# Kernel tuning notes

Measured on AMD Instinct MI355X. Metric: run time of the kernel, lower is better.

Reference implementation:

```python
import jax, jax.numpy as jnp
import numpy as np
import math

D_MODEL = 1024
D_STATE = 16
D_CONV = 4
EXPAND = 2
D_INNER = EXPAND * D_MODEL  # 2048
DT_RANK = math.ceil(D_MODEL / 16)  # 64
BATCH = 4
SEQLEN = 4096


def setup_inputs() -> dict:
    key = jax.random.key(0)
    ks = jax.random.split(key, 8)
    sc = lambda d: 1.0 / np.sqrt(d)
    hidden_states = jax.random.normal(ks[0], (BATCH, SEQLEN, D_MODEL), jnp.float32)
    in_proj_w = jax.random.normal(ks[1], (2 * D_INNER, D_MODEL), jnp.float32) * sc(D_MODEL)
    conv_w = jax.random.normal(ks[2], (D_INNER, 1, D_CONV), jnp.float32) * sc(D_CONV)
    conv_b = jnp.zeros((D_INNER,), jnp.float32)
    x_proj_w = jax.random.normal(ks[3], (DT_RANK + 2 * D_STATE, D_INNER), jnp.float32) * sc(D_INNER)
    dt_init_std = DT_RANK ** -0.5
    dt_proj_w = jax.random.uniform(ks[4], (D_INNER, DT_RANK), jnp.float32, -dt_init_std, dt_init_std)
    # dt bias init: inverse-softplus of dt sampled log-uniform in [1e-3, 1e-1]
    dt = jnp.exp(jax.random.uniform(ks[5], (D_INNER,), jnp.float32)
                 * (math.log(0.1) - math.log(0.001)) + math.log(0.001))
    dt = jnp.clip(dt, 1e-4, None)
    dt_proj_b = dt + jnp.log(-jnp.expm1(-dt))
    A_log = jnp.log(jnp.tile(jnp.arange(1, D_STATE + 1, dtype=jnp.float32), (D_INNER, 1)))
    Dp = jnp.ones((D_INNER,), jnp.float32)
    out_proj_w = jax.random.normal(ks[6], (D_MODEL, D_INNER), jnp.float32) * sc(D_INNER)
    return {
        'hidden_states': hidden_states,
        'in_proj_w': in_proj_w,
        'conv_w': conv_w,
        'conv_b': conv_b,
        'x_proj_w': x_proj_w,
        'dt_proj_w': dt_proj_w,
        'dt_proj_b': dt_proj_b,
        'A_log': A_log,
        'D': Dp,
        'out_proj_w': out_proj_w,
    }


def _bimamba_fwd(hidden_states, in_proj_w, conv_w, conv_b, x_proj_w,
                 dt_proj_w, dt_proj_b, A_log, D, out_proj_w):
    Bb, L, _ = hidden_states.shape
    # 1) input projection, split into x and gate z
    xz = hidden_states @ in_proj_w.T                      # (B, L, 2*d_inner)
    x, z = jnp.split(xz, 2, axis=-1)
    # 2) causal depthwise conv1d (torch pads d_conv-1 both sides then truncates
    #    to L, equivalent to left-pad d_conv-1)
    xc = x.transpose(0, 2, 1)                             # (B, d_inner, L)
    xc = jax.lax.conv_general_dilated(
        xc, conv_w, window_strides=(1,), padding=[(D_CONV - 1, 0)],
        dimension_numbers=('NCH', 'OIH', 'NCH'), feature_group_count=D_INNER)
    xc = xc + conv_b[None, :, None]
    x = jax.nn.silu(xc.transpose(0, 2, 1))                # (B, L, d_inner)
    # 3) input-dependent SSM parameters
    x_dbl = x @ x_proj_w.T                                # (B, L, dt_rank + 2*d_state)
    dt, Bm, Cm = jnp.split(x_dbl, [DT_RANK, DT_RANK + D_STATE], axis=-1)
    dt = jax.nn.softplus(dt @ dt_proj_w.T + dt_proj_b)    # (B, L, d_inner)
    A = -jnp.exp(A_log)                                   # (d_inner, d_state)

    # 4) selective scan (faithful to source: einsum 'bdn,bdk->bdk' sums dA over
    #    the state dim n and scales h by that scalar per (b,d))
    def step(h, inp):
        dt_t, B_t, C_t, x_t = inp                         # (B,d),(B,n),(B,n),(B,d)
        dtc = jnp.clip(dt_t, -10.0, 10.0)
        dA = jnp.exp(jnp.clip(dtc[..., None] * A[None], -50.0, 50.0))  # (B,d,n)
        dB_x = dtc[..., None] * B_t[:, None, :] * jnp.clip(x_t, -10.0, 10.0)[..., None]
        h_new = jnp.clip(dA.sum(-1, keepdims=True) * h + dB_x, -100.0, 100.0)
        y_t = (h_new * C_t[:, None, :]).sum(-1)           # (B, d_inner)
        return h_new, y_t

    h0 = jnp.zeros((Bb, D_INNER, D_STATE), x.dtype)
    xs = (dt.transpose(1, 0, 2), Bm.transpose(1, 0, 2),
          Cm.transpose(1, 0, 2), x.transpose(1, 0, 2))
    _, ys = jax.lax.scan(step, h0, xs)                    # ys: (L, B, d_inner)
    y = ys.transpose(1, 0, 2) + x * D[None, None, :]
    # 5) gate + output projection
    y = y * jax.nn.silu(z)
    return y @ out_proj_w.T                               # (B, L, d_model)


def reference(hidden_states, in_proj_w, conv_w, conv_b, x_proj_w,
              dt_proj_w, dt_proj_b, A_log, D, out_proj_w):
    return _bimamba_fwd(hidden_states, in_proj_w, conv_w, conv_b, x_proj_w,
                        dt_proj_w, dt_proj_b, A_log, D, out_proj_w)
```

## Files before the change

kernel.cpp:

```cpp
#include <hip/hip_runtime.h>
#include <math.h>

#define B_   4
#define L_   4096
#define DM   1024
#define DI   2048
#define M_   (B_ * L_)
#define NT   32
#define CH   16
#define NCHUNK (L_ / NT)

typedef unsigned short u16;
typedef unsigned int   u32;
typedef __attribute__((ext_vector_type(8))) short s16x8;
typedef __attribute__((ext_vector_type(4))) float f32x4;

__device__ __forceinline__ float clampf(float v, float lo, float hi) {
    return fminf(fmaxf(v, lo), hi);
}
__device__ __forceinline__ float b2f(u32 u) {
    union { u32 i; float f; } v; v.i = u << 16; return v.f;
}
__device__ __forceinline__ u16 f2b(float f) {
    union { float f; u32 i; } v; v.f = f;
    u32 r = v.i + 0x7FFFu + ((v.i >> 16) & 1u);
    return (u16)(r >> 16);
}
__device__ __forceinline__ float siluf(float x) {
    return x / (1.f + __expf(-x));
}
__device__ __forceinline__ float xor1_add(float x) {
    int t = __builtin_amdgcn_mov_dpp(__float_as_int(x), 0xB1, 0xF, 0xF, true);
    return x + __int_as_float(t);
}
__device__ __forceinline__ float xor2_add(float x) {
    int t = __builtin_amdgcn_mov_dpp(__float_as_int(x), 0x4E, 0xF, 0xF, true);
    return x + __int_as_float(t);
}
__device__ __forceinline__ float mirror8_add(float x) {
    int t = __builtin_amdgcn_mov_dpp(__float_as_int(x), 0x141, 0xF, 0xF, true);
    return x + __int_as_float(t);
}

__global__ __launch_bounds__(256) void gemm_inproj_mfma(
    const float* __restrict__ A, const float* __restrict__ Bw,
    float* __restrict__ X, u16* __restrict__ ZS)
{
    __shared__ u16 Ah[128 * 40], Al[128 * 40], Bh[128 * 40], Bl[128 * 40];
    const int K = 1024;
    const int tid = threadIdx.x;
    const int wid = tid >> 6, lane = tid & 63;
    const int wm = wid >> 1, wn = wid & 1;
    const int lr = lane & 15, lk = (lane >> 4) * 8;
    const long m0 = (long)blockIdx.x * 128;
    const int n0 = blockIdx.y * 128;
    const int srr = tid >> 3;
    const int skk = (tid & 7) * 4;

    f32x4 acc[4][4];
#pragma unroll
    for (int m = 0; m < 4; ++m)
#pragma unroll
        for (int n = 0; n < 4; ++n) acc[m][n] = (f32x4){0.f, 0.f, 0.f, 0.f};

    for (int k0 = 0; k0 < K; k0 += 32) {
        float4 ta[4], tb[4];
#pragma unroll
        for (int v = 0; v < 4; ++v) {
            ta[v] = *(const float4*)&A[(m0 + v * 32 + srr) * K + k0 + skk];
            tb[v] = *(const float4*)&Bw[((long)n0 + v * 32 + srr) * K + k0 + skk];
        }
        __syncthreads();
#pragma unroll
        for (int v = 0; v < 4; ++v) {
            int off = (v * 32 + srr) * 40 + skk;
            ushort4 h, l;
            h.x = f2b(ta[v].x); l.x = f2b(ta[v].x - b2f(h.x));
            h.y = f2b(ta[v].y); l.y = f2b(ta[v].y - b2f(h.y));
            h.z = f2b(ta[v].z); l.z = f2b(ta[v].z - b2f(h.z));
            h.w = f2b(ta[v].w); l.w = f2b(ta[v].w - b2f(h.w));
            *(ushort4*)&Ah[off] = h; *(ushort4*)&Al[off] = l;
            h.x = f2b(tb[v].x); l.x = f2b(tb[v].x - b2f(h.x));
            h.y = f2b(tb[v].y); l.y = f2b(tb[v].y - b2f(h.y));
            h.z = f2b(tb[v].z); l.z = f2b(tb[v].z - b2f(h.z));
            h.w = f2b(tb[v].w); l.w = f2b(tb[v].w - b2f(h.w));
            *(ushort4*)&Bh[off] = h; *(ushort4*)&Bl[off] = l;
        }
        __syncthreads();
        s16x8 ah[4], al[4], bh[4], bl[4];
#pragma unroll
        for (int m = 0; m < 4; ++m) {
            int ro = (wm * 64 + m * 16 + lr) * 40 + lk;
            ah[m] = *(const s16x8*)&Ah[ro];
            al[m] = *(const s16x8*)&Al[ro];
        }
#pragma unroll
        for (int n = 0; n < 4; ++n) {
            int ro = (wn * 64 + n * 16 + lr) * 40 + lk;
            bh[n] = *(const s16x8*)&Bh[ro];
            bl[n] = *(const s16x8*)&Bl[ro];
        }
#pragma unroll
        for (int m = 0; m < 4; ++m)
#pragma unroll
            for (int n = 0; n < 4; ++n) {
                acc[m][n] = __builtin_amdgcn_mfma_f32_16x16x32_bf16(ah[m], bh[n], acc[m][n], 0, 0, 0);
                acc[m][n] = __builtin_amdgcn_mfma_f32_16x16x32_bf16(ah[m], bl[n], acc[m][n], 0, 0, 0);
                acc[m][n] = __builtin_amdgcn_mfma_f32_16x16x32_bf16(al[m], bh[n], acc[m][n], 0, 0, 0);
            }
    }

    const int rbase = (lane >> 4) * 4;
    if (n0 < DI) {
#pragma unroll
        for (int m = 0; m < 4; ++m) {
            long row = m0 + wm * 64 + m * 16 + rbase;
#pragma unroll
            for (int n = 0; n < 4; ++n) {
                int col = n0 + wn * 64 + n * 16 + lr;
#pragma unroll
                for (int ri = 0; ri < 4; ++ri)
                    X[(row + ri) * DI + col] = acc[m][n][ri];
            }
        }
    } else {
#pragma unroll
        for (int m = 0; m < 4; ++m) {
            long row = m0 + wm * 64 + m * 16 + rbase;
#pragma unroll
            for (int n = 0; n < 4; ++n) {
                int col = n0 - DI + wn * 64 + n * 16 + lr;
#pragma unroll
                for (int ri = 0; ri < 4; ++ri)
                    ZS[(row + ri) * DI + col] = f2b(siluf(acc[m][n][ri]));
            }
        }
    }
}

__global__ __launch_bounds__(256) void gemm_outproj_mfma(
    const float* __restrict__ A, const float* __restrict__ Bw,
    float* __restrict__ C)
{
    __shared__ u16 Ah[128 * 40], Bh[128 * 40];
    const int K = 2048;
    const int tid = threadIdx.x;
    const int wid = tid >> 6, lane = tid & 63;
    const int wm = wid >> 1, wn = wid & 1;
    const int lr = lane & 15, lk = (lane >> 4) * 8;
    const long m0 = (long)blockIdx.x * 128;
    const int n0 = blockIdx.y * 128;
    const int srr = tid >> 3;
    const int skk = (tid & 7) * 4;

    f32x4 acc[4][4];
#pragma unroll
    for (int m = 0; m < 4; ++m)
#pragma unroll
        for (int n = 0; n < 4; ++n) acc[m][n] = (f32x4){0.f, 0.f, 0.f, 0.f};

    for (int k0 = 0; k0 < K; k0 += 32) {
        float4 ta[4], tb[4];
#pragma unroll
        for (int v = 0; v < 4; ++v) {
            ta[v] = *(const float4*)&A[(m0 + v * 32 + srr) * K + k0 + skk];
            tb[v] = *(const float4*)&Bw[((long)n0 + v * 32 + srr) * K + k0 + skk];
        }
        __syncthreads();
#pragma unroll
        for (int v = 0; v < 4; ++v) {
            int off = (v * 32 + srr) * 40 + skk;
            ushort4 h;
            h.x = f2b(ta[v].x); h.y = f2b(ta[v].y);
            h.z = f2b(ta[v].z); h.w = f2b(ta[v].w);
            *(ushort4*)&Ah[off] = h;
            h.x = f2b(tb[v].x); h.y = f2b(tb[v].y);
            h.z = f2b(tb[v].z); h.w = f2b(tb[v].w);
            *(ushort4*)&Bh[off] = h;
        }
        __syncthreads();
        s16x8 ah[4], bh[4];
#pragma unroll
        for (int m = 0; m < 4; ++m)
            ah[m] = *(const s16x8*)&Ah[(wm * 64 + m * 16 + lr) * 40 + lk];
#pragma unroll
        for (int n = 0; n < 4; ++n)
            bh[n] = *(const s16x8*)&Bh[(wn * 64 + n * 16 + lr) * 40 + lk];
#pragma unroll
        for (int m = 0; m < 4; ++m)
#pragma unroll
            for (int n = 0; n < 4; ++n)
                acc[m][n] = __builtin_amdgcn_mfma_f32_16x16x32_bf16(ah[m], bh[n], acc[m][n], 0, 0, 0);
    }

    const int rbase = (lane >> 4) * 4;
#pragma unroll
    for (int m = 0; m < 4; ++m) {
        long row = m0 + wm * 64 + m * 16 + rbase;
#pragma unroll
        for (int n = 0; n < 4; ++n) {
            int col = n0 + wn * 64 + n * 16 + lr;
#pragma unroll
            for (int ri = 0; ri < 4; ++ri)
                C[(row + ri) * DM + col] = acc[m][n][ri];
        }
    }
}

__global__ __launch_bounds__(256) void gemm_xproj_conv_mfma(
    const float* __restrict__ X, const float* __restrict__ convw,
    const float* __restrict__ convb, const float* __restrict__ Bw,
    float* __restrict__ C)
{
    const int PITCH = 72;
    __shared__ u16 Ah[64 * PITCH], Al[64 * PITCH];
    __shared__ u16 Bh[96 * PITCH], Bl[96 * PITCH];
    const int tid = threadIdx.x;
    const int wid = tid >> 6, lane = tid & 63;
    const int wm = wid >> 1, wn = wid & 1;
    const int lr = lane & 15, lk = (lane >> 4) * 8;
    const long m0 = (long)blockIdx.x * 64;

    const int rg = tid >> 6;
    const int kk = tid & 63;
    const long gr0 = m0 + rg * 16;
    const int l0r = (int)(gr0 & (L_ - 1));

    f32x4 acc[2][3];
#pragma unroll
    for (int m = 0; m < 2; ++m)
#pragma unroll
        for (int n = 0; n < 3; ++n) acc[m][n] = (f32x4){0.f, 0.f, 0.f, 0.f};

    for (int k0 = 0; k0 < DI; k0 += 64) {
        float4 cwv = *(const float4*)&convw[(k0 + kk) * 4];
        float cbv = convb[k0 + kk];
        float xm3, xm2, xm1;
        if (l0r == 0) { xm3 = 0.f; xm2 = 0.f; xm1 = 0.f; }
        else {
            xm3 = X[(gr0 - 3) * DI + k0 + kk];
            xm2 = X[(gr0 - 2) * DI + k0 + kk];
            xm1 = X[(gr0 - 1) * DI + k0 + kk];
        }
        __syncthreads();
#pragma unroll
// ... 25 lines not shown
            h = f2b(t.w); Bh[off + 3] = h; Bl[off + 3] = f2b(t.w - b2f(h));
        }
        __syncthreads();
#pragma unroll
        for (int kf = 0; kf < 2; ++kf) {
            s16x8 ah[2], al[2], bh[3], bl[3];
#pragma unroll
            for (int m = 0; m < 2; ++m) {
                int ro = (wm * 32 + m * 16 + lr) * PITCH + kf * 32 + lk;
                ah[m] = *(const s16x8*)&Ah[ro];
                al[m] = *(const s16x8*)&Al[ro];
            }
#pragma unroll
            for (int n = 0; n < 3; ++n) {
                int ro = (wn * 48 + n * 16 + lr) * PITCH + kf * 32 + lk;
                bh[n] = *(const s16x8*)&Bh[ro];
                bl[n] = *(const s16x8*)&Bl[ro];
            }
#pragma unroll
            for (int m = 0; m < 2; ++m)
#pragma unroll
                for (int n = 0; n < 3; ++n) {
                    acc[m][n] = __builtin_amdgcn_mfma_f32_16x16x32_bf16(ah[m], bh[n], acc[m][n], 0, 0, 0);
                    acc[m][n] = __builtin_amdgcn_mfma_f32_16x16x32_bf16(ah[m], bl[n], acc[m][n], 0, 0, 0);
                    acc[m][n] = __builtin_amdgcn_mfma_f32_16x16x32_bf16(al[m], bh[n], acc[m][n], 0, 0, 0);
                }
        }
    }

    const int rbase = (lane >> 4) * 4;
#pragma unroll
    for (int m = 0; m < 2; ++m) {
        long row = m0 + wm * 32 + m * 16 + rbase;
#pragma unroll
        for (int n = 0; n < 3; ++n) {
            int col = wn * 48 + n * 16 + lr;
#pragma unroll
            for (int ri = 0; ri < 4; ++ri)
                C[(row + ri) * 96 + col] = acc[m][n][ri];
        }
    }
}

__global__ __launch_bounds__(256, 1) void scan_kernel(
    float* xg, const u16* __restrict__ zsg, const float* __restrict__ xdbl,
    const float* __restrict__ dtw, const float* __restrict__ dtb,
    const float* __restrict__ Dv, const float* __restrict__ convw,
    const float* __restrict__ convb)
{
    __shared__ float sa [3][NT][CH + 1];
    __shared__ float ssv[3][NT][CH + 1];
    __shared__ float sxa[3][NT][CH + 1];
    __shared__ u16   szs[3][NT][CH + 1];
    __shared__ float sbc[3][NT][36];
    __shared__ float sxr[2][NT][CH + 1];
    __shared__ float sdt[2][NT][68];
    __shared__ float scarry[3][CH];
    __shared__ float sg[2][NT][CH + 1];

    const int tid = threadIdx.x;
    const int bb   = blockIdx.x >> 7;
    const int cgrp = blockIdx.x & 127;
    const int d0 = cgrp * CH;
    const long lrow0 = (long)bb * L_;
    const bool producer = (tid >= 128);

    if (producer && (tid - 128) < 3 * CH) {
        int pi = tid - 128;
        scarry[pi >> 4][pi & 15] = 0.f;
    }

    const int p  = tid & 127;
    const int ch = p >> 3, q = p & 7;
    const int d  = d0 + ch;
    float4 cw = {0,0,0,0};
    float cbd = 0.f, dtbd = 0.f, Dd = 0.f;
    float4 wv[16];
    if (producer) {
#pragma unroll
        for (int g = 0; g < 16; ++g)
            wv[g] = *(const float4*)&dtw[(long)d * 64 + 4 * g];
        cw  = *(const float4*)&convw[d * 4];
        cbd = convb[d];
        dtbd = dtb[d];
    } else {
        Dd = Dv[d];
        __builtin_amdgcn_s_setprio(1);
    }
    const int srow = p >> 2, sc4 = (p & 3) * 4;

    auto STAGE = [&](int cc) {
        const long lr0 = lrow0 + (long)cc * NT;
        const int spr = cc & 1, cbn = cc % 3;
        {
            long go = (lr0 + srow) * DI + d0 + sc4;
            float4 xv = *(const float4*)&xg[go];
            sxr[spr][srow][sc4 + 0] = xv.x; sxr[spr][srow][sc4 + 1] = xv.y;
            sxr[spr][srow][sc4 + 2] = xv.z; sxr[spr][srow][sc4 + 3] = xv.w;
            ushort4 zv = *(const ushort4*)&zsg[go];
            szs[cbn][srow][sc4 + 0] = zv.x; szs[cbn][srow][sc4 + 1] = zv.y;
            szs[cbn][srow][sc4 + 2] = zv.z; szs[cbn][srow][sc4 + 3] = zv.w;
        }
#pragma unroll
        for (int v = 0; v < 4; ++v) {
            int idx = p + v * 128;
            int row = idx >> 4, c4 = (idx & 15) * 4;
            float4 t = *(const float4*)&xdbl[(lr0 + row) * 96 + c4];
            *(float4*)&sdt[spr][row][c4] = t;
        }
#pragma unroll
        for (int v = 0; v < 2; ++v) {
            int idx = p + v * 128;
            int row = idx >> 3, sj = idx & 7;
            if (sj < 4) {
                float4 bv = *(const float4*)&xdbl[(lr0 + row) * 96 + 64 + sj * 4];
                sbc[cbn][row][8 * sj + 0] = bv.x; sbc[cbn][row][8 * sj + 2] = bv.y;
                sbc[cbn][row][8 * sj + 4] = bv.z; sbc[cbn][row][8 * sj + 6] = bv.w;
            } else {
                int jj = sj - 4;
                float4 cv = *(const float4*)&xdbl[(lr0 + row) * 96 + 80 + jj * 4];
                sbc[cbn][row][8 * jj + 1] = cv.x; sbc[cbn][row][8 * jj + 3] = cv.y;
                sbc[cbn][row][8 * jj + 5] = cv.z; sbc[cbn][row][8 * jj + 7] = cv.w;
            }
        }
    };

    auto COMPUTE = [&](int cc) {
        const int spr = cc & 1, cbn = cc % 3;
        float xw0, xw1, xw2;
        if (q == 0) { xw0 = scarry[0][ch]; xw1 = scarry[1][ch]; xw2 = scarry[2][ch]; }
        else { xw0 = sxr[spr][4 * q - 3][ch]; xw1 = sxr[spr][4 * q - 2][ch];
               xw2 = sxr[spr][4 * q - 1][ch]; }
        float xw3 = sxr[spr][4 * q + 0][ch];
        float xw4 = sxr[spr][4 * q + 1][ch];
        float xw5 = sxr[spr][4 * q + 2][ch];
        float xw6 = sxr[spr][4 * q + 3][ch];
        sxa[cbn][4 * q + 0][ch] =
            siluf(fmaf(xw0, cw.x, fmaf(xw1, cw.y, fmaf(xw2, cw.z, fmaf(xw3, cw.w, cbd)))));
        sxa[cbn][4 * q + 1][ch] =
            siluf(fmaf(xw1, cw.x, fmaf(xw2, cw.y, fmaf(xw3, cw.z, fmaf(xw4, cw.w, cbd)))));
        sxa[cbn][4 * q + 2][ch] =
            siluf(fmaf(xw2, cw.x, fmaf(xw3, cw.y, fmaf(xw4, cw.z, fmaf(xw5, cw.w, cbd)))));
        sxa[cbn][4 * q + 3][ch] =
            siluf(fmaf(xw3, cw.x, fmaf(xw4, cw.y, fmaf(xw5, cw.z, fmaf(xw6, cw.w, cbd)))));
        if (q == 0) {
            scarry[0][ch] = sxr[spr][NT - 3][ch];
            scarry[1][ch] = sxr[spr][NT - 2][ch];
            scarry[2][ch] = sxr[spr][NT - 1][ch];
        }
#pragma unroll
        for (int j = 0; j < 4; ++j) {
            const int stp = 8 * j + q;
            const float* row = &sdt[spr][stp][0];
            float a0 = 0.f, a1 = 0.f, a2 = 0.f, a3 = 0.f;
#pragma unroll
            for (int g = 0; g < 4; ++g) {
                float4 u0 = *(const float4*)(row + 16 * g + 0);
                float4 u1 = *(const float4*)(row + 16 * g + 4);
                float4 u2 = *(const float4*)(row + 16 * g + 8);
                float4 u3 = *(const float4*)(row + 16 * g + 12);
                float4 w0 = wv[4 * g + 0], w1 = wv[4 * g + 1];
                float4 w2 = wv[4 * g + 2], w3 = wv[4 * g + 3];
                a0 = fmaf(u0.x, w0.x, a0); a0 = fmaf(u0.y, w0.y, a0);
                a0 = fmaf(u0.z, w0.z, a0); a0 = fmaf(u0.w, w0.w, a0);
                a1 = fmaf(u1.x, w1.x, a1); a1 = fmaf(u1.y, w1.y, a1);
                a1 = fmaf(u1.z, w1.z, a1); a1 = fmaf(u1.w, w1.w, a1);
                a2 = fmaf(u2.x, w2.x, a2); a2 = fmaf(u2.y, w2.y, a2);
                a2 = fmaf(u2.z, w2.z, a2); a2 = fmaf(u2.w, w2.w, a2);
                a3 = fmaf(u3.x, w3.x, a3); a3 = fmaf(u3.y, w3.y, a3);
                a3 = fmaf(u3.z, w3.z, a3); a3 = fmaf(u3.w, w3.w, a3);
            }
            float dt = ((a0 + a1) + (a2 + a3)) + dtbd;
            float sp = fmaxf(dt, 0.f) + __logf(1.f + __expf(-fabsf(dt)));
            float dtc = fminf(sp, 10.f);
            float r = __expf(-dtc);
            float r2 = r * r, r4 = r2 * r2, r8 = r4 * r4;
            float a = r * (1.f + r) * (1.f + r2) * (1.f + r4) * (1.f + r8);
            float sv = dtc * clampf(sxa[cbn][stp][ch], -10.f, 10.f);
            sa [cbn][stp][ch] = a;
            ssv[cbn][stp][ch] = sv;
        }
    };

    __syncthreads();
    if (producer) STAGE(0);
    __syncthreads();
    if (producer) { STAGE(1); COMPUTE(0); }
    __syncthreads();

    float h0 = 0.f, h1 = 0.f;
    for (int k = 0; k < NCHUNK; ++k) {
        if (!producer) {
            if (k > 0) {
                const long lp0 = lrow0 + (long)(k - 1) * NT;
                const int pgb = (k - 1) & 1;
                float4 gv;
                gv.x = sg[pgb][srow][sc4 + 0]; gv.y = sg[pgb][srow][sc4 + 1];
                gv.z = sg[pgb][srow][sc4 + 2]; gv.w = sg[pgb][srow][sc4 + 3];
                *(float4*)&xg[(lp0 + srow) * DI + d0 + sc4] = gv;
            }
            const int cb = k % 3, gb = k & 1;
            const float (*pa)[CH + 1]  = sa[cb];
            const float (*psv)[CH + 1] = ssv[cb];
            const float (*pxa)[CH + 1] = sxa[cb];
            const u16   (*pzs)[CH + 1] = szs[cb];
            const float (*pbc)[36]     = sbc[cb];
#pragma unroll 4
            for (int stp = 0; stp < NT; ++stp) {
                float a  = pa[stp][ch];
                float sv = psv[stp][ch];
                float4 bc = *(const float4*)&pbc[stp][4 * q];
                h0 = clampf(fmaf(a, h0, sv * bc.x), -100.f, 100.f);
                h1 = clampf(fmaf(a, h1, sv * bc.z), -100.f, 100.f);
                float yp = fmaf(h0, bc.y, h1 * bc.w);
                yp = xor1_add(yp);
                yp = xor2_add(yp);
                yp = mirror8_add(yp);
                if (q == 0)
                    sg[gb][stp][ch] = fmaf(pxa[stp][ch], Dd, yp) * b2f(pzs[stp][ch]);
            }
        } else {
            if (k + 2 < NCHUNK) STAGE(k + 2);
            if (k + 1 < NCHUNK) COMPUTE(k + 1);
        }
        __syncthreads();
    }
    if (!producer) {
        const long lp0 = lrow0 + (long)(NCHUNK - 1) * NT;
        const int pgb = (NCHUNK - 1) & 1;
        float4 gv;
        gv.x = sg[pgb][srow][sc4 + 0]; gv.y = sg[pgb][srow][sc4 + 1];
        gv.z = sg[pgb][srow][sc4 + 2]; gv.w = sg[pgb][srow][sc4 + 3];
        *(float4*)&xg[(lp0 + srow) * DI + d0 + sc4] = gv;
    }
}

extern "C" void kernel_launch(void* const* d_in, const int* in_sizes, int n_in,
                              void* d_out, int out_size, void* d_ws, size_t ws_size,
                              hipStream_t stream)
{
    const float* hidden = (const float*)d_in[0];
    const float* in_w   = (const float*)d_in[1];
    const float* conv_w = (const float*)d_in[2];
    const float* conv_b = (const float*)d_in[3];
    const float* xprj_w = (const float*)d_in[4];
    const float* dtw    = (const float*)d_in[5];
    const float* dtb    = (const float*)d_in[6];
    const float* Dv     = (const float*)d_in[8];
    const float* outw   = (const float*)d_in[9];
    float* out = (float*)d_out;

    const size_t MD = (size_t)M_ * DI;
    float* xbuf = (float*)d_ws;
    u16*   zsbuf = (u16*)(xbuf + MD);
    float* xdbl = (float*)(zsbuf + MD);
    const size_t need = MD * sizeof(float) + MD * sizeof(u16)
                      + (size_t)M_ * 96 * sizeof(float);
    if (ws_size < need) return;

    {
        dim3 g(M_ / 128, 4096 / 128);
        gemm_inproj_mfma<<<g, 256, 0, stream>>>(hidden, in_w, xbuf, zsbuf);
    }
    gemm_xproj_conv_mfma<<<M_ / 64, 256, 0, stream>>>(
        xbuf, conv_w, conv_b, xprj_w, xdbl);
    scan_kernel<<<512, 256, 0, stream>>>(
        xbuf, zsbuf, xdbl, dtw, dtb, Dv, conv_w, conv_b);
    {
        dim3 g(M_ / 128, 1024 / 128);
        gemm_outproj_mfma<<<g, 256, 0, stream>>>(xbuf, outw, out);
    }
}
```

Baseline: 1.352 ms.

## Split selective scan into time segments with per-segment dt, z, scan and outproj kernels

The monolithic scan kernel, with its producer/consumer warps computing conv, dt projection and state updates, is replaced by a loop over 512-step time segments. Each segment runs separate kernels: conv+silu prep, an MFMA dt-projection GEMM with softplus, a z-projection GEMM with silu, a register-streamed scan that carries state between segments, and the output projection. B and C are written transposed (C in bf16) so the scan reads them contiguously. The goal is to move the dt projection onto matrix cores, keep per-segment buffers cache-resident and raise scan parallelism. In exchange it adds many small launches and repeated global round trips per segment.

```diff
diff --git a/kernel.cpp b/kernel.cpp
--- a/kernel.cpp
+++ b/kernel.cpp
@@ -6,9 +6,9 @@
 #define DM   1024
 #define DI   2048
 #define M_   (B_ * L_)
-#define NT   32
-#define CH   16
-#define NCHUNK (L_ / NT)
+#define TS_  512
+#define NSEG (L_ / TS_)
+#define NCK  (TS_ / 16)
 
 typedef unsigned short u16;
 typedef unsigned int   u32;
@@ -29,6 +29,8 @@
 __device__ __forceinline__ float siluf(float x) {
     return x / (1.f + __expf(-x));
 }
+#define LOF(w) __uint_as_float((u32)(w) << 16)
+#define HIF(w) __uint_as_float((u32)(w) & 0xffff0000u)
 __device__ __forceinline__ float xor1_add(float x) {
     int t = __builtin_amdgcn_mov_dpp(__float_as_int(x), 0xB1, 0xF, 0xF, true);
     return x + __int_as_float(t);
@@ -42,9 +44,9 @@
     return x + __int_as_float(t);
 }
 
-__global__ __launch_bounds__(256) void gemm_inproj_mfma(
+__global__ __launch_bounds__(256) void gemm_inproj_x(
     const float* __restrict__ A, const float* __restrict__ Bw,
-    float* __restrict__ X, u16* __restrict__ ZS)
+    float* __restrict__ X)
 {
     __shared__ u16 Ah[128 * 40], Al[128 * 40], Bh[128 * 40], Bl[128 * 40];
     const int K = 1024;
@@ -111,89 +113,6 @@
     }
 
     const int rbase = (lane >> 4) * 4;
-    if (n0 < DI) {
-#pragma unroll
-        for (int m = 0; m < 4; ++m) {
-            long row = m0 + wm * 64 + m * 16 + rbase;
-#pragma unroll
-            for (int n = 0; n < 4; ++n) {
-                int col = n0 + wn * 64 + n * 16 + lr;
-#pragma unroll
-                for (int ri = 0; ri < 4; ++ri)
-                    X[(row + ri) * DI + col] = acc[m][n][ri];
-            }
-        }
-    } else {
-#pragma unroll
-        for (int m = 0; m < 4; ++m) {
-            long row = m0 + wm * 64 + m * 16 + rbase;
-#pragma unroll
-            for (int n = 0; n < 4; ++n) {
-                int col = n0 - DI + wn * 64 + n * 16 + lr;
-#pragma unroll
-                for (int ri = 0; ri < 4; ++ri)
-                    ZS[(row + ri) * DI + col] = f2b(siluf(acc[m][n][ri]));
-            }
-        }
-    }
-}
-
-__global__ __launch_bounds__(256) void gemm_outproj_mfma(
-    const float* __restrict__ A, const float* __restrict__ Bw,
-    float* __restrict__ C)
-{
-    __shared__ u16 Ah[128 * 40], Bh[128 * 40];
-    const int K = 2048;
-    const int tid = threadIdx.x;
-    const int wid = tid >> 6, lane = tid & 63;
-    const int wm = wid >> 1, wn = wid & 1;
-    const int lr = lane & 15, lk = (lane >> 4) * 8;
-    const long m0 = (long)blockIdx.x * 128;
-    const int n0 = blockIdx.y * 128;
-    const int srr = tid >> 3;
-    const int skk = (tid & 7) * 4;
-
-    f32x4 acc[4][4];
-#pragma unroll
-    for (int m = 0; m < 4; ++m)
-#pragma unroll
-        for (int n = 0; n < 4; ++n) acc[m][n] = (f32x4){0.f, 0.f, 0.f, 0.f};
-
-    for (int k0 = 0; k0 < K; k0 += 32) {
-        float4 ta[4], tb[4];
-#pragma unroll
-        for (int v = 0; v < 4; ++v) {
-            ta[v] = *(const float4*)&A[(m0 + v * 32 + srr) * K + k0 + skk];
-            tb[v] = *(const float4*)&Bw[((long)n0 + v * 32 + srr) * K + k0 + skk];
-        }
-        __syncthreads();
-#pragma unroll
-        for (int v = 0; v < 4; ++v) {
-            int off = (v * 32 + srr) * 40 + skk;
-            ushort4 h;
-            h.x = f2b(ta[v].x); h.y = f2b(ta[v].y);
-            h.z = f2b(ta[v].z); h.w = f2b(ta[v].w);
-            *(ushort4*)&Ah[off] = h;
-            h.x = f2b(tb[v].x); h.y = f2b(tb[v].y);
-            h.z = f2b(tb[v].z); h.w = f2b(tb[v].w);
-            *(ushort4*)&Bh[off] = h;
-        }
-        __syncthreads();
-        s16x8 ah[4], bh[4];
-#pragma unroll
-        for (int m = 0; m < 4; ++m)
-            ah[m] = *(const s16x8*)&Ah[(wm * 64 + m * 16 + lr) * 40 + lk];
-#pragma unroll
-        for (int n = 0; n < 4; ++n)
-            bh[n] = *(const s16x8*)&Bh[(wn * 64 + n * 16 + lr) * 40 + lk];
-#pragma unroll
-        for (int m = 0; m < 4; ++m)
-#pragma unroll
-            for (int n = 0; n < 4; ++n)
-                acc[m][n] = __builtin_amdgcn_mfma_f32_16x16x32_bf16(ah[m], bh[n], acc[m][n], 0, 0, 0);
-    }
-
-    const int rbase = (lane >> 4) * 4;
 #pragma unroll
     for (int m = 0; m < 4; ++m) {
         long row = m0 + wm * 64 + m * 16 + rbase;
@@ -202,7 +121,7 @@
             int col = n0 + wn * 64 + n * 16 + lr;
 #pragma unroll
             for (int ri = 0; ri < 4; ++ri)
-                C[(row + ri) * DM + col] = acc[m][n][ri];
+                X[(row + ri) * DI + col] = acc[m][n][ri];
         }
     }
 }
@@ -210,7 +129,7 @@
 __global__ __launch_bounds__(256) void gemm_xproj_conv_mfma(
     const float* __restrict__ X, const float* __restrict__ convw,
     const float* __restrict__ convb, const float* __restrict__ Bw,
-    float* __restrict__ C)
+    float* __restrict__ XD, float* __restrict__ BT, u16* __restrict__ CT)
 {
     const int PITCH = 72;
     __shared__ u16 Ah[64 * PITCH], Al[64 * PITCH];
@@ -302,206 +221,418 @@
 #pragma unroll
     for (int m = 0; m < 2; ++m) {
         long row = m0 + wm * 32 + m * 16 + rbase;
+        int b = (int)(row >> 12);
+        int t = (int)(row & (L_ - 1));
 #pragma unroll
         for (int n = 0; n < 3; ++n) {
             int col = wn * 48 + n * 16 + lr;
+            if (col < 64) {
+#pragma unroll
+                for (int ri = 0; ri < 4; ++ri)
+                    XD[(row + ri) * 64 + col] = acc[m][n][ri];
+            } else if (col < 80) {
+                int nn = col - 64;
+                float4 bv;
+                bv.x = acc[m][n][0]; bv.y = acc[m][n][1];
+                bv.z = acc[m][n][2]; bv.w = acc[m][n][3];
+                *(float4*)&BT[((long)(b * 16 + nn)) * L_ + t] = bv;
+            } else {
+                int nn = col - 80;
+                ushort4 pk;
+                pk.x = f2b(acc[m][n][0]); pk.y = f2b(acc[m][n][1]);
+                pk.z = f2b(acc[m][n][2]); pk.w = f2b(acc[m][n][3]);
+                *(ushort4*)&CT[((long)(b * 16 + nn)) * L_ + t] = pk;
+            }
+        }
+    }
+}
+
+__global__ __launch_bounds__(256) void prep_seg(
+    const float* __restrict__ X, const float* __restrict__ convw,
+    const float* __restrict__ convb, float* __restrict__ XAT, int ts)
+{
+    const int tid = threadIdx.x;
+    const int dl = tid & 63, tseg = tid >> 6;
+    const int d = blockIdx.x * 64 + dl;
+    const int t0 = ts + blockIdx.y * 32 + tseg * 8;
+    const int b = blockIdx.z;
+    const long xb = ((long)b * L_ + t0) * DI + d;
+
+    float4 cw = *(const float4*)&convw[d * 4];
+    float cb = convb[d];
+    float xm3, xm2, xm1;
+    if (t0 == 0) { xm3 = 0.f; xm2 = 0.f; xm1 = 0.f; }
+    else {
+        xm3 = X[xb - 3 * DI];
+        xm2 = X[xb - 2 * DI];
+        xm1 = X[xb - 1 * DI];
+    }
+    float xa[8];
+#pragma unroll
+    for (int i = 0; i < 8; ++i) {
+        float x0 = X[xb + (long)i * DI];
+        float v = cb;
+        v = fmaf(xm3, cw.x, v);
+        v = fmaf(xm2, cw.y, v);
+        v = fmaf(xm1, cw.z, v);
+        v = fmaf(x0,  cw.w, v);
+        xa[i] = siluf(v);
+        xm3 = xm2; xm2 = xm1; xm1 = x0;
+    }
+    float* o = &XAT[((long)(b * DI + d)) * TS_ + (t0 - ts)];
+    *(float4*)o       = (float4){xa[0], xa[1], xa[2], xa[3]};
+    *(float4*)(o + 4) = (float4){xa[4], xa[5], xa[6], xa[7]};
+}
+
+__global__ __launch_bounds__(256) void gemm_dtproj_seg(
+    const float* __restrict__ XD, const float* __restrict__ Wdt,
+    const float* __restrict__ dtb, float* __restrict__ DTC, int ts)
+{
+    const int PITCH = 72;
+    __shared__ u16 Ah[128 * PITCH], Al[128 * PITCH];
+    __shared__ u16 Bh[128 * PITCH], Bl[128 * PITCH];
+    const int tid = threadIdx.x;
+    const int wid = tid >> 6, lane = tid & 63;
+    const int wm = wid >> 1, wn = wid & 1;
+    const int lr = lane & 15;
+    const int bb = blockIdx.x >> 2, rr = blockIdx.x & 3;
+    const long m0 = (long)bb * L_ + ts + rr * 128;
+    const int n0 = blockIdx.y * 128;
+
+#pragma unroll
+    for (int v = 0; v < 8; ++v) {
+        int i = tid + v * 256;
+        int r = i >> 4, c4 = (i & 15) * 4;
+        float4 ta = *(const float4*)&XD[(m0 + r) * 64 + c4];
+        float4 tb = *(const float4*)&Wdt[((long)n0 + r) * 64 + c4];
+        int off = r * PITCH + c4;
+        u16 h;
+        h = f2b(ta.x); Ah[off + 0] = h; Al[off + 0] = f2b(ta.x - b2f(h));
+        h = f2b(ta.y); Ah[off + 1] = h; Al[off + 1] = f2b(ta.y - b2f(h));
+        h = f2b(ta.z); Ah[off + 2] = h; Al[off + 2] = f2b(ta.z - b2f(h));
+        h = f2b(ta.w); Ah[off + 3] = h; Al[off + 3] = f2b(ta.w - b2f(h));
+        h = f2b(tb.x); Bh[off + 0] = h; Bl[off + 0] = f2b(tb.x - b2f(h));
+        h = f2b(tb.y); Bh[off + 1] = h; Bl[off + 1] = f2b(tb.y - b2f(h));
+        h = f2b(tb.z); Bh[off + 2] = h; Bl[off + 2] = f2b(tb.z - b2f(h));
+        h = f2b(tb.w); Bh[off + 3] = h; Bl[off + 3] = f2b(tb.w - b2f(h));
+    }
+    __syncthreads();
+
+    f32x4 acc[4][4];
+#pragma unroll
+    for (int m = 0; m < 4; ++m)
+#pragma unroll
+        for (int n = 0; n < 4; ++n) acc[m][n] = (f32x4){0.f, 0.f, 0.f, 0.f};
+
+#pragma unroll
+    for (int kf = 0; kf < 2; ++kf) {
+        const int lk = kf * 32 + (lane >> 4) * 8;
+        s16x8 ah[4], al[4], bh[4], bl[4];
+#pragma unroll
+        for (int m = 0; m < 4; ++m) {
+            int ro = (wm * 64 + m * 16 + lr) * PITCH + lk;
+            ah[m] = *(const s16x8*)&Ah[ro];
+            al[m] = *(const s16x8*)&Al[ro];
+        }
+#pragma unroll
+        for (int n = 0; n < 4; ++n) {
+            int ro = (wn * 64 + n * 16 + lr) * PITCH + lk;
+            bh[n] = *(const s16x8*)&Bh[ro];
+            bl[n] = *(const s16x8*)&Bl[ro];
+        }
+#pragma unroll
+        for (int m = 0; m < 4; ++m)
+#pragma unroll
+            for (int n = 0; n < 4; ++n) {
+                acc[m][n] = __builtin_amdgcn_mfma_f32_16x16x32_bf16(ah[m], bh[n], acc[m][n], 0, 0, 0);
+                acc[m][n] = __builtin_amdgcn_mfma_f32_16x16x32_bf16(ah[m], bl[n], acc[m][n], 0, 0, 0);
+                acc[m][n] = __builtin_amdgcn_mfma_f32_16x16x32_bf16(al[m], bh[n], acc[m][n], 0, 0, 0);
+            }
+    }
+
+    const int rbase = (lane >> 4) * 4;
+#pragma unroll
+    for (int n = 0; n < 4; ++n) {
+        int d = n0 + wn * 64 + n * 16 + lr;
+        float bias = dtb[d];
+#pragma unroll
+        for (int m = 0; m < 4; ++m) {
+            long row = m0 + wm * 64 + m * 16 + rbase;
+            int tt = (int)(row & (L_ - 1)) - ts;
+            float4 pk;
+#pragma unroll
+            for (int ri = 0; ri < 4; ++ri) {
+                float dt = acc[m][n][ri] + bias;
+                float sp = fmaxf(dt, 0.f) + __logf(1.f + __expf(-fabsf(dt)));
+                ((float*)&pk)[ri] = fminf(sp, 10.f);
+            }
+            *(float4*)&DTC[((long)(bb * DI + d)) * TS_ + tt] = pk;
+        }
+    }
+}
+
+__global__ __launch_bounds__(256) void gemm_zproj_seg(
+    const float* __restrict__ A, const float* __restrict__ Bw,
+    u16* __restrict__ ZS, int ts)
+{
+    __shared__ u16 Ah[128 * 40], Bh[128 * 40];
+    const int K = 1024;
+    const int tid = threadIdx.x;
+    const int wid = tid >> 6, lane = tid & 63;
+    const int wm = wid >> 1, wn = wid & 1;
+    const int lr = lane & 15, lk = (lane >> 4) * 8;
+    const int bb = blockIdx.x >> 2, rr = blockIdx.x & 3;
+    const long m0 = (long)bb * L_ + ts + rr * 128;
+    const int n0 = blockIdx.y * 128 + DI;
+    const int srr = tid >> 3;
+    const int skk = (tid & 7) * 4;
+
+    f32x4 acc[4][4];
+#pragma unroll
+    for (int m = 0; m < 4; ++m)
+#pragma unroll
+        for (int n = 0; n < 4; ++n) acc[m][n] = (f32x4){0.f, 0.f, 0.f, 0.f};
+
+    for (int k0 = 0; k0 < K; k0 += 32) {
+        float4 ta[4], tb[4];
+#pragma unroll
+        for (int v = 0; v < 4; ++v) {
+            ta[v] = *(const float4*)&A[(m0 + v * 32 + srr) * K + k0 + skk];
+            tb[v] = *(const float4*)&Bw[((long)n0 + v * 32 + srr) * K + k0 + skk];
+        }
+        __syncthreads();
+#pragma unroll
+        for (int v = 0; v < 4; ++v) {
+            int off = (v * 32 + srr) * 40 + skk;
+            ushort4 h;
+            h.x = f2b(ta[v].x); h.y = f2b(ta[v].y);
+            h.z = f2b(ta[v].z); h.w = f2b(ta[v].w);
+            *(ushort4*)&Ah[off] = h;
+            h.x = f2b(tb[v].x); h.y = f2b(tb[v].y);
+            h.z = f2b(tb[v].z); h.w = f2b(tb[v].w);
+            *(ushort4*)&Bh[off] = h;
+        }
+        __syncthreads();
+        s16x8 ah[4], bh[4];
+#pragma unroll
+        for (int m = 0; m < 4; ++m)
+            ah[m] = *(const s16x8*)&Ah[(wm * 64 + m * 16 + lr) * 40 + lk];
+#pragma unroll
+        for (int n = 0; n < 4; ++n)
+            bh[n] = *(const s16x8*)&Bh[(wn * 64 + n * 16 + lr) * 40 + lk];
+#pragma unroll
+        for (int m = 0; m < 4; ++m)
+#pragma unroll
+            for (int n = 0; n < 4; ++n)
+                acc[m][n] = __builtin_amdgcn_mfma_f32_16x16x32_bf16(ah[m], bh[n], acc[m][n], 0, 0, 0);
+    }
+
+    const int rbase = (lane >> 4) * 4;
+#pragma unroll
+    for (int m = 0; m < 4; ++m) {
+        long row = m0 + wm * 64 + m * 16 + rbase;
+        int tt = (int)(row & (L_ - 1)) - ts;
+#pragma unroll
+        for (int n = 0; n < 4; ++n) {
+            int d = (n0 - DI) + wn * 64 + n * 16 + lr;
+            ushort4 pk;
+            pk.x = f2b(siluf(acc[m][n][0]));
+            pk.y = f2b(siluf(acc[m][n][1]));
+            pk.z = f2b(siluf(acc[m][n][2]));
+            pk.w = f2b(siluf(acc[m][n][3]));
+            *(ushort4*)&ZS[((long)(bb * DI + d)) * TS_ + tt] = pk;
+        }
+    }
+}
+
+struct SBuf {
+    float4 dt0, dt1, dt2, dt3;
+    float4 xa0, xa1, xa2, xa3;
+    float4 b00, b01, b02, b03;
+    float4 b10, b11, b12, b13;
+    uint4  c0a, c0b, c1a, c1b;
+};
+
+__global__ __launch_bounds__(256) void scan_seg(
+    float* dtu, const float* __restrict__ xat, const float* __restrict__ BT,
+    const u16* __restrict__ CT, const float* __restrict__ Dv,
+    float* __restrict__ HC, int ts, int first)
+{
+    const int tid = threadIdx.x;
+    const int l = tid & 63, w = tid >> 6;
+    const int c = l >> 3, q = l & 7;
+    const int s = blockIdx.x * 32 + w * 8 + c;
+    const int d = s & (DI - 1);
+    const int b = s >> 11;
+    const float Dd = Dv[d];
+    const long sb = (long)s * TS_;
+    const long pB0 = ((long)(b * 16 + 2 * q)) * L_ + ts;
+    const long pB1 = pB0 + L_;
+
+    float h0 = 0.f, h1 = 0.f;
+    if (!first) {
+        float2 hv = *(const float2*)&HC[(long)s * 16 + 2 * q];
+        h0 = hv.x; h1 = hv.y;
+    }
+
+    auto LOAD = [&](int cc, SBuf& S) {
+        long o = (long)cc * 16;
+        S.dt0 = *(const float4*)&dtu[sb + o];      S.dt1 = *(const float4*)&dtu[sb + o + 4];
+        S.dt2 = *(const float4*)&dtu[sb + o + 8];  S.dt3 = *(const float4*)&dtu[sb + o + 12];
+        S.xa0 = *(const float4*)&xat[sb + o];      S.xa1 = *(const float4*)&xat[sb + o + 4];
+        S.xa2 = *(const float4*)&xat[sb + o + 8];  S.xa3 = *(const float4*)&xat[sb + o + 12];
+        S.b00 = *(const float4*)&BT[pB0 + o];      S.b01 = *(const float4*)&BT[pB0 + o + 4];
+        S.b02 = *(const float4*)&BT[pB0 + o + 8];  S.b03 = *(const float4*)&BT[pB0 + o + 12];
+        S.b10 = *(const float4*)&BT[pB1 + o];      S.b11 = *(const float4*)&BT[pB1 + o + 4];
+        S.b12 = *(const float4*)&BT[pB1 + o + 8];  S.b13 = *(const float4*)&BT[pB1 + o + 12];
+        S.c0a = *(const uint4*)&CT[pB0 + o];       S.c0b = *(const uint4*)&CT[pB0 + o + 8];
+        S.c1a = *(const uint4*)&CT[pB1 + o];       S.c1b = *(const uint4*)&CT[pB1 + o + 8];
+    };
+
+    auto ONE = [&](float dtc, float xav, float B0v, float B1v,
+                   float C0v, float C1v) -> float {
+        float r = __expf(-dtc);
+        float r2 = r * r, r4 = r2 * r2, r8 = r4 * r4;
+        float a = r * (1.f + r) * (1.f + r2) * (1.f + r4) * (1.f + r8);
+        float sv = dtc * clampf(xav, -10.f, 10.f);
+        h0 = clampf(fmaf(a, h0, sv * B0v), -100.f, 100.f);
+        h1 = clampf(fmaf(a, h1, sv * B1v), -100.f, 100.f);
+        float y = fmaf(h0, C0v, h1 * C1v);
+        y = xor1_add(y);
+        y = xor2_add(y);
+        y = mirror8_add(y);
+        return fmaf(xav, Dd, y);
+    };
+
+    auto COMPUTE = [&](int cc, const SBuf& S) {
+        float4 u0, u1, u2, u3;
+        u0.x = ONE(S.dt0.x, S.xa0.x, S.b00.x, S.b10.x, LOF(S.c0a.x), LOF(S.c1a.x));
+        u0.y = ONE(S.dt0.y, S.xa0.y, S.b00.y, S.b10.y, HIF(S.c0a.x), HIF(S.c1a.x));
+        u0.z = ONE(S.dt0.z, S.xa0.z, S.b00.z, S.b10.z, LOF(S.c0a.y), LOF(S.c1a.y));
+        u0.w = ONE(S.dt0.w, S.xa0.w, S.b00.w, S.b10.w, HIF(S.c0a.y), HIF(S.c1a.y));
+        u1.x = ONE(S.dt1.x, S.xa1.x, S.b01.x, S.b11.x, LOF(S.c0a.z), LOF(S.c1a.z));
+        u1.y = ONE(S.dt1.y, S.xa1.y, S.b01.y, S.b11.y, HIF(S.c0a.z), HIF(S.c1a.z));
+        u1.z = ONE(S.dt1.z, S.xa1.z, S.b01.z, S.b11.z, LOF(S.c0a.w), LOF(S.c1a.w));
+        u1.w = ONE(S.dt1.w, S.xa1.w, S.b01.w, S.b11.w, HIF(S.c0a.w), HIF(S.c1a.w));
+        u2.x = ONE(S.dt2.x, S.xa2.x, S.b02.x, S.b12.x, LOF(S.c0b.x), LOF(S.c1b.x));
+        u2.y = ONE(S.dt2.y, S.xa2.y, S.b02.y, S.b12.y, HIF(S.c0b.x), HIF(S.c1b.x));
+        u2.z = ONE(S.dt2.z, S.xa2.z, S.b02.z, S.b12.z, LOF(S.c0b.y), LOF(S.c1b.y));
+        u2.w = ONE(S.dt2.w, S.xa2.w, S.b02.w, S.b12.w, HIF(S.c0b.y), HIF(S.c1b.y));
+        u3.x = ONE(S.dt3.x, S.xa3.x, S.b03.x, S.b13.x, LOF(S.c0b.z), LOF(S.c1b.z));
+        u3.y = ONE(S.dt3.y, S.xa3.y, S.b03.y, S.b13.y, HIF(S.c0b.z), HIF(S.c1b.z));
+        u3.z = ONE(S.dt3.z, S.xa3.z, S.b03.z, S.b13.z, LOF(S.c0b.w), LOF(S.c1b.w));
+        u3.w = ONE(S.dt3.w, S.xa3.w, S.b03.w, S.b13.w, HIF(S.c0b.w), HIF(S.c1b.w));
+        if (q == 0) {
+            long o = (long)cc * 16;
+            *(float4*)&dtu[sb + o]      = u0;
+            *(float4*)&dtu[sb + o + 4]  = u1;
+            *(float4*)&dtu[sb + o + 8]  = u2;
+            *(float4*)&dtu[sb + o + 12] = u3;
+        }
+    };
+
+    SBuf A, Bf;
+    LOAD(0, A);
+    for (int k = 0; k < NCK; k += 2) {
+        LOAD(k + 1, Bf);
+        COMPUTE(k, A);
+        int k2 = (k + 2 < NCK) ? k + 2 : NCK - 1;
+        LOAD(k2, A);
+        COMPUTE(k + 1, Bf);
+    }
+    *(float2*)&HC[(long)s * 16 + 2 * q] = (float2){h0, h1};
+}
+
+__global__ __launch_bounds__(256) void gemm_outproj_seg(
+    const float* __restrict__ U, const u16* __restrict__ ZS,
+    const float* __restrict__ Bw, float* __restrict__ C, int ts)
+{
+    __shared__ u16 Ah[128 * 40], Bh[128 * 40];
+    const int K = 2048;
+    const int tid = threadIdx.x;
+    const int wid = tid >> 6, lane = tid & 63;
+    const int wm = wid >> 1, wn = wid & 1;
+    const int lr = lane & 15, lk = (lane >> 4) * 8;
+    const int bb = blockIdx.x >> 2, rr = blockIdx.x & 3;
+    const long m0 = (long)bb * L_ + ts + rr * 128;
+    const int tt0 = rr * 128;
+    const int n0 = blockIdx.y * 128;
+    const int srr = tid >> 3;
+    const int skk = (tid & 7) * 4;
+    const int kkA = tid & 31, msegA = tid >> 5;
+
+    f32x4 acc[4][4];
+#pragma unroll
+    for (int m = 0; m < 4; ++m)
+#pragma unroll
+        for (int n = 0; n < 4; ++n) acc[m][n] = (f32x4){0.f, 0.f, 0.f, 0.f};
+
+    for (int k0 = 0; k0 < K; k0 += 32) {
+        const long abase = ((long)(bb * DI) + k0 + kkA) * TS_ + tt0 + msegA * 16;
+        float4 ua0 = *(const float4*)&U[abase];
+        float4 ua1 = *(const float4*)&U[abase + 4];
+        float4 ua2 = *(const float4*)&U[abase + 8];
+        float4 ua3 = *(const float4*)&U[abase + 12];
+        uint4 za = *(const uint4*)&ZS[abase];
+        uint4 zb = *(const uint4*)&ZS[abase + 8];
+        float4 tb[4];
+#pragma unroll
+        for (int v = 0; v < 4; ++v)
+            tb[v] = *(const float4*)&Bw[((long)n0 + v * 32 + srr) * K + k0 + skk];
+        __syncthreads();
+        {
+            int mb = msegA * 16;
+            Ah[(mb + 0) * 40 + kkA]  = f2b(ua0.x * LOF(za.x));
+            Ah[(mb + 1) * 40 + kkA]  = f2b(ua0.y * HIF(za.x));
+            Ah[(mb + 2) * 40 + kkA]  = f2b(ua0.z * LOF(za.y));
+            Ah[(mb + 3) * 40 + kkA]  = f2b(ua0.w * HIF(za.y));
+            Ah[(mb + 4) * 40 + kkA]  = f2b(ua1.x * LOF(za.z));
+            Ah[(mb + 5) * 40 + kkA]  = f2b(ua1.y * HIF(za.z));
+            Ah[(mb + 6) * 40 + kkA]  = f2b(ua1.z * LOF(za.w));
+            Ah[(mb + 7) * 40 + kkA]  = f2b(ua1.w * HIF(za.w));
+            Ah[(mb + 8) * 40 + kkA]  = f2b(ua2.x * LOF(zb.x));
+            Ah[(mb + 9) * 40 + kkA]  = f2b(ua2.y * HIF(zb.x));
+            Ah[(mb + 10) * 40 + kkA] = f2b(ua2.z * LOF(zb.y));
+            Ah[(mb + 11) * 40 + kkA] = f2b(ua2.w * HIF(zb.y));
+            Ah[(mb + 12) * 40 + kkA] = f2b(ua3.x * LOF(zb.z));
+            Ah[(mb + 13) * 40 + kkA] = f2b(ua3.y * HIF(zb.z));
+            Ah[(mb + 14) * 40 + kkA] = f2b(ua3.z * LOF(zb.w));
+            Ah[(mb + 15) * 40 + kkA] = f2b(ua3.w * HIF(zb.w));
+        }
+#pragma unroll
+        for (int v = 0; v < 4; ++v) {
+            int off = (v * 32 + srr) * 40 + skk;
+            ushort4 h;
+            h.x = f2b(tb[v].x); h.y = f2b(tb[v].y);
+            h.z = f2b(tb[v].z); h.w = f2b(tb[v].w);
+            *(ushort4*)&Bh[off] = h;
+        }
+        __syncthreads();
+        s16x8 ah[4], bh[4];
+#pragma unroll
+        for (int m = 0; m < 4; ++m)
+            ah[m] = *(const s16x8*)&Ah[(wm * 64 + m * 16 + lr) * 40 + lk];
+#pragma unroll
+        for (int n = 0; n < 4; ++n)
+            bh[n] = *(const s16x8*)&Bh[(wn * 64 + n * 16 + lr) * 40 + lk];
+#pragma unroll
+        for (int m = 0; m < 4; ++m)
+#pragma unroll
+            for (int n = 0; n < 4; ++n)
+                acc[m][n] = __builtin_amdgcn_mfma_f32_16x16x32_bf16(ah[m], bh[n], acc[m][n], 0, 0, 0);
+    }
+
+    const int rbase = (lane >> 4) * 4;
+#pragma unroll
+    for (int m = 0; m < 4; ++m) {
+        long row = m0 + wm * 64 + m * 16 + rbase;
+#pragma unroll
+        for (int n = 0; n < 4; ++n) {
+            int col = n0 + wn * 64 + n * 16 + lr;
 #pragma unroll
             for (int ri = 0; ri < 4; ++ri)
-                C[(row + ri) * 96 + col] = acc[m][n][ri];
-        }
-    }
-}
-
-__global__ __launch_bounds__(256, 1) void scan_kernel(
-    float* xg, const u16* __restrict__ zsg, const float* __restrict__ xdbl,
-    const float* __restrict__ dtw, const float* __restrict__ dtb,
-    const float* __restrict__ Dv, const float* __restrict__ convw,
-    const float* __restrict__ convb)
-{
-    __shared__ float sa [3][NT][CH + 1];
-    __shared__ float ssv[3][NT][CH + 1];
-    __shared__ float sxa[3][NT][CH + 1];
-    __shared__ u16   szs[3][NT][CH + 1];
-    __shared__ float sbc[3][NT][36];
-    __shared__ float sxr[2][NT][CH + 1];
-    __shared__ float sdt[2][NT][68];
-    __shared__ float scarry[3][CH];
-    __shared__ float sg[2][NT][CH + 1];
-
-    const int tid = threadIdx.x;
-    const int bb   = blockIdx.x >> 7;
-    const int cgrp = blockIdx.x & 127;
-    const int d0 = cgrp * CH;
-    const long lrow0 = (long)bb * L_;
-    const bool producer = (tid >= 128);
-
-    if (producer && (tid - 128) < 3 * CH) {
-        int pi = tid - 128;
-        scarry[pi >> 4][pi & 15] = 0.f;
-    }
-
-    const int p  = tid & 127;
-    const int ch = p >> 3, q = p & 7;
-    const int d  = d0 + ch;
-    float4 cw = {0,0,0,0};
-    float cbd = 0.f, dtbd = 0.f, Dd = 0.f;
-    float4 wv[16];
-    if (producer) {
-#pragma unroll
-        for (int g = 0; g < 16; ++g)
-            wv[g] = *(const float4*)&dtw[(long)d * 64 + 4 * g];
-        cw  = *(const float4*)&convw[d * 4];
-        cbd = convb[d];
-        dtbd = dtb[d];
-    } else {
-        Dd = Dv[d];
-        __builtin_amdgcn_s_setprio(1);
-    }
-    const int srow = p >> 2, sc4 = (p & 3) * 4;
-
-    auto STAGE = [&](int cc) {
-        const long lr0 = lrow0 + (long)cc * NT;
-        const int spr = cc & 1, cbn = cc % 3;
-        {
-            long go = (lr0 + srow) * DI + d0 + sc4;
-            float4 xv = *(const float4*)&xg[go];
-            sxr[spr][srow][sc4 + 0] = xv.x; sxr[spr][srow][sc4 + 1] = xv.y;
-            sxr[spr][srow][sc4 + 2] = xv.z; sxr[spr][srow][sc4 + 3] = xv.w;
-            ushort4 zv = *(const ushort4*)&zsg[go];
-            szs[cbn][srow][sc4 + 0] = zv.x; szs[cbn][srow][sc4 + 1] = zv.y;
-            szs[cbn][srow][sc4 + 2] = zv.z; szs[cbn][srow][sc4 + 3] = zv.w;
-        }
-#pragma unroll
-        for (int v = 0; v < 4; ++v) {
-            int idx = p + v * 128;
-            int row = idx >> 4, c4 = (idx & 15) * 4;
-            float4 t = *(const float4*)&xdbl[(lr0 + row) * 96 + c4];
-            *(float4*)&sdt[spr][row][c4] = t;
-        }
-#pragma unroll
-        for (int v = 0; v < 2; ++v) {
-            int idx = p + v * 128;
-            int row = idx >> 3, sj = idx & 7;
-            if (sj < 4) {
-                float4 bv = *(const float4*)&xdbl[(lr0 + row) * 96 + 64 + sj * 4];
-                sbc[cbn][row][8 * sj + 0] = bv.x; sbc[cbn][row][8 * sj + 2] = bv.y;
-                sbc[cbn][row][8 * sj + 4] = bv.z; sbc[cbn][row][8 * sj + 6] = bv.w;
-            } else {
-                int jj = sj - 4;
-                float4 cv = *(const float4*)&xdbl[(lr0 + row) * 96 + 80 + jj * 4];
-                sbc[cbn][row][8 * jj + 1] = cv.x; sbc[cbn][row][8 * jj + 3] = cv.y;
-                sbc[cbn][row][8 * jj + 5] = cv.z; sbc[cbn][row][8 * jj + 7] = cv.w;
-            }
-        }
-    };
-
-    auto COMPUTE = [&](int cc) {
-        const int spr = cc & 1, cbn = cc % 3;
-        float xw0, xw1, xw2;
-        if (q == 0) { xw0 = scarry[0][ch]; xw1 = scarry[1][ch]; xw2 = scarry[2][ch]; }
-        else { xw0 = sxr[spr][4 * q - 3][ch]; xw1 = sxr[spr][4 * q - 2][ch];
-               xw2 = sxr[spr][4 * q - 1][ch]; }
-        float xw3 = sxr[spr][4 * q + 0][ch];
-        float xw4 = sxr[spr][4 * q + 1][ch];
-        float xw5 = sxr[spr][4 * q + 2][ch];
-        float xw6 = sxr[spr][4 * q + 3][ch];
-        sxa[cbn][4 * q + 0][ch] =
-            siluf(fmaf(xw0, cw.x, fmaf(xw1, cw.y, fmaf(xw2, cw.z, fmaf(xw3, cw.w, cbd)))));
-        sxa[cbn][4 * q + 1][ch] =
-            siluf(fmaf(xw1, cw.x, fmaf(xw2, cw.y, fmaf(xw3, cw.z, fmaf(xw4, cw.w, cbd)))));
-        sxa[cbn][4 * q + 2][ch] =
-            siluf(fmaf(xw2, cw.x, fmaf(xw3, cw.y, fmaf(xw4, cw.z, fmaf(xw5, cw.w, cbd)))));
-        sxa[cbn][4 * q + 3][ch] =
-            siluf(fmaf(xw3, cw.x, fmaf(xw4, cw.y, fmaf(xw5, cw.z, fmaf(xw6, cw.w, cbd)))));
-        if (q == 0) {
-            scarry[0][ch] = sxr[spr][NT - 3][ch];
-            scarry[1][ch] = sxr[spr][NT - 2][ch];
-            scarry[2][ch] = sxr[spr][NT - 1][ch];
-        }
-#pragma unroll
-        for (int j = 0; j < 4; ++j) {
-            const int stp = 8 * j + q;
-            const float* row = &sdt[spr][stp][0];
-            float a0 = 0.f, a1 = 0.f, a2 = 0.f, a3 = 0.f;
-#pragma unroll
-            for (int g = 0; g < 4; ++g) {
-                float4 u0 = *(const float4*)(row + 16 * g + 0);
-                float4 u1 = *(const float4*)(row + 16 * g + 4);
-                float4 u2 = *(const float4*)(row + 16 * g + 8);
-                float4 u3 = *(const float4*)(row + 16 * g + 12);
-                float4 w0 = wv[4 * g + 0], w1 = wv[4 * g + 1];
-                float4 w2 = wv[4 * g + 2], w3 = wv[4 * g + 3];
-                a0 = fmaf(u0.x, w0.x, a0); a0 = fmaf(u0.y, w0.y, a0);
-                a0 = fmaf(u0.z, w0.z, a0); a0 = fmaf(u0.w, w0.w, a0);
-                a1 = fmaf(u1.x, w1.x, a1); a1 = fmaf(u1.y, w1.y, a1);
-                a1 = fmaf(u1.z, w1.z, a1); a1 = fmaf(u1.w, w1.w, a1);
-                a2 = fmaf(u2.x, w2.x, a2); a2 = fmaf(u2.y, w2.y, a2);
-                a2 = fmaf(u2.z, w2.z, a2); a2 = fmaf(u2.w, w2.w, a2);
-                a3 = fmaf(u3.x, w3.x, a3); a3 = fmaf(u3.y, w3.y, a3);
-                a3 = fmaf(u3.z, w3.z, a3); a3 = fmaf(u3.w, w3.w, a3);
-            }
-            float dt = ((a0 + a1) + (a2 + a3)) + dtbd;
-            float sp = fmaxf(dt, 0.f) + __logf(1.f + __expf(-fabsf(dt)));
-            float dtc = fminf(sp, 10.f);
-            float r = __expf(-dtc);
-            float r2 = r * r, r4 = r2 * r2, r8 = r4 * r4;
-            float a = r * (1.f + r) * (1.f + r2) * (1.f + r4) * (1.f + r8);
-            float sv = dtc * clampf(sxa[cbn][stp][ch], -10.f, 10.f);
-            sa [cbn][stp][ch] = a;
-            ssv[cbn][stp][ch] = sv;
-        }
-    };
-
-    __syncthreads();
-    if (producer) STAGE(0);
-    __syncthreads();
-    if (producer) { STAGE(1); COMPUTE(0); }
-    __syncthreads();
-
-    float h0 = 0.f, h1 = 0.f;
-    for (int k = 0; k < NCHUNK; ++k) {
-        if (!producer) {
-            if (k > 0) {
-                const long lp0 = lrow0 + (long)(k - 1) * NT;
-                const int pgb = (k - 1) & 1;
-                float4 gv;
-                gv.x = sg[pgb][srow][sc4 + 0]; gv.y = sg[pgb][srow][sc4 + 1];
-                gv.z = sg[pgb][srow][sc4 + 2]; gv.w = sg[pgb][srow][sc4 + 3];
-                *(float4*)&xg[(lp0 + srow) * DI + d0 + sc4] = gv;
-            }
-            const int cb = k % 3, gb = k & 1;
-            const float (*pa)[CH + 1]  = sa[cb];
-            const float (*psv)[CH + 1] = ssv[cb];
-            const float (*pxa)[CH + 1] = sxa[cb];
-            const u16   (*pzs)[CH + 1] = szs[cb];
-            const float (*pbc)[36]     = sbc[cb];
-#pragma unroll 4
-            for (int stp = 0; stp < NT; ++stp) {
-                float a  = pa[stp][ch];
-                float sv = psv[stp][ch];
-                float4 bc = *(const float4*)&pbc[stp][4 * q];
-                h0 = clampf(fmaf(a, h0, sv * bc.x), -100.f, 100.f);
-                h1 = clampf(fmaf(a, h1, sv * bc.z), -100.f, 100.f);
-                float yp = fmaf(h0, bc.y, h1 * bc.w);
-                yp = xor1_add(yp);
-                yp = xor2_add(yp);
-                yp = mirror8_add(yp);
-                if (q == 0)
-                    sg[gb][stp][ch] = fmaf(pxa[stp][ch], Dd, yp) * b2f(pzs[stp][ch]);
-            }
-        } else {
-            if (k + 2 < NCHUNK) STAGE(k + 2);
-            if (k + 1 < NCHUNK) COMPUTE(k + 1);
-        }
-        __syncthreads();
-    }
-    if (!producer) {
-        const long lp0 = lrow0 + (long)(NCHUNK - 1) * NT;
-        const int pgb = (NCHUNK - 1) & 1;
-        float4 gv;
-        gv.x = sg[pgb][srow][sc4 + 0]; gv.y = sg[pgb][srow][sc4 + 1];
-        gv.z = sg[pgb][srow][sc4 + 2]; gv.w = sg[pgb][srow][sc4 + 3];
-        *(float4*)&xg[(lp0 + srow) * DI + d0 + sc4] = gv;
+                C[(row + ri) * DM + col] = acc[m][n][ri];
+        }
     }
 }
 
@@ -521,23 +652,35 @@
     float* out = (float*)d_out;
 
     const size_t MD = (size_t)M_ * DI;
-    float* xbuf = (float*)d_ws;
-    u16*   zsbuf = (u16*)(xbuf + MD);
-    float* xdbl = (float*)(zsbuf + MD);
-    const size_t need = MD * sizeof(float) + MD * sizeof(u16)
-                      + (size_t)M_ * 96 * sizeof(float);
+    const size_t SEG = (size_t)B_ * TS_ * DI;
+    float* xbuf  = (float*)d_ws;
+    float* xdblD = xbuf + MD;
+    float* BT    = xdblD + (size_t)M_ * 64;
+    u16*   CT    = (u16*)(BT + (size_t)B_ * 16 * L_);
+    float* dtu   = (float*)(CT + (size_t)B_ * 16 * L_);
+    float* xaseg = dtu + SEG;
+    u16*   zsseg = (u16*)(xaseg + SEG);
+    float* hc    = (float*)(zsseg + SEG);
+    const size_t need = MD * 4 + (size_t)M_ * 64 * 4
+                      + (size_t)B_ * 16 * L_ * 6
+                      + SEG * 4 + SEG * 4 + SEG * 2
+                      + (size_t)B_ * DI * 16 * 4;
     if (ws_size < need) return;
 
-    {
-        dim3 g(M_ / 128, 4096 / 128);
-        gemm_inproj_mfma<<<g, 256, 0, stream>>>(hidden, in_w, xbuf, zsbuf);
-    }
+    gemm_inproj_x<<<dim3(M_ / 128, 16), 256, 0, stream>>>(hidden, in_w, xbuf);
     gemm_xproj_conv_mfma<<<M_ / 64, 256, 0, stream>>>(
-        xbuf, conv_w, conv_b, xprj_w, xdbl);
-    scan_kernel<<<512, 256, 0, stream>>>(
-        xbuf, zsbuf, xdbl, dtw, dtb, Dv, conv_w, conv_b);
-    {
-        dim3 g(M_ / 128, 1024 / 128);
-        gemm_outproj_mfma<<<g, 256, 0, stream>>>(xbuf, outw, out);
-    }
-}
+        xbuf, conv_w, conv_b, xprj_w, xdblD, BT, CT);
+    for (int s = 0; s < NSEG; ++s) {
+        int ts = s * TS_;
+        prep_seg<<<dim3(DI / 64, TS_ / 32, B_), 256, 0, stream>>>(
+            xbuf, conv_w, conv_b, xaseg, ts);
+        gemm_dtproj_seg<<<dim3(16, 16), 256, 0, stream>>>(
+            xdblD, dtw, dtb, dtu, ts);
+        gemm_zproj_seg<<<dim3(16, 16), 256, 0, stream>>>(
+            hidden, in_w, zsseg, ts);
+        scan_seg<<<256, 256, 0, stream>>>(
+            dtu, xaseg, BT, CT, Dv, hc, ts, s == 0);
+        gemm_outproj_seg<<<dim3(16, 8), 256, 0, stream>>>(
+            dtu, zsseg, outw, out, ts);
+    }
+}
```

Result: slower. 2.201 ms (+62.8%).
